# Kernel optimization log

Measured on AMD Instinct MI355X. Metric: run time of the kernel, lower is better.

Reference implementation:

```python
import jax, jax.numpy as jnp
import numpy as np

N = 4_194_304        # total nodes in the batch
NUM_GRAPHS = 32_768  # number of graphs (segments)
VOCAB = 100          # Embedding(100, 1)

# Wigner-3j contraction constants (real basis)
C01 = float(1.0 / np.sqrt(3.0))   # 0e x 1e -> 1e and 1e x 0e -> 1e
C11 = float(1.0 / np.sqrt(6.0))   # 1e x 1e -> 1e (Levi-Civita / sqrt(6))
# path weights: sqrt(ir_out.dim / fan_in_paths); 3 paths -> 1.0, 2 paths -> sqrt(3/2)
PW1 = 1.0
PW2 = float(np.sqrt(1.5))


def setup_inputs() -> dict:
    key = jax.random.key(0)
    ks = jax.random.split(key, 12)
    z = jax.random.randint(ks[0], (N,), 0, VOCAB, dtype=jnp.int32)
    pos = jax.random.normal(ks[1], (N, 3), dtype=jnp.float32)
    batch = jnp.sort(jax.random.randint(ks[2], (N,), 0, NUM_GRAPHS, dtype=jnp.int32))
    embed_table = jax.random.normal(ks[3], (VOCAB, 1), dtype=jnp.float32)
    lin_w = jax.random.normal(ks[4], (3, 3), dtype=jnp.float32) / np.sqrt(3.0)
    lin_b = jax.random.normal(ks[5], (3,), dtype=jnp.float32) * 0.1
    tp1_w = jax.random.normal(ks[6], (3,), dtype=jnp.float32)   # 3 CG paths
    tp2_w = jax.random.normal(ks[7], (2,), dtype=jnp.float32)   # 2 CG paths
    tp3_w = jax.random.normal(ks[8], (2,), dtype=jnp.float32)
    gate_w = jax.random.normal(ks[9], (2,), dtype=jnp.float32)
    fc_w = jax.random.normal(ks[10], (3, 3), dtype=jnp.float32) / np.sqrt(3.0)
    fc_b = jax.random.normal(ks[11], (3,), dtype=jnp.float32) * 0.1
    return {"z": z, "pos": pos, "batch": batch, "embed_table": embed_table,
            "lin_w": lin_w, "lin_b": lin_b, "tp1_w": tp1_w, "tp2_w": tp2_w,
            "tp3_w": tp3_w, "gate_w": gate_w, "fc_w": fc_w, "fc_b": fc_b}


def reference(z, pos, batch, embed_table, lin_w, lin_b, tp1_w, tp2_w, tp3_w, gate_w, fc_w, fc_b):
    # node features: x = [scalar embedding s (0e), transformed position v (1e)]
    s = embed_table[z][:, 0]                      # [N]
    v = pos @ lin_w.T + lin_b                     # [N, 3]
    sv = s[:, None] * v                           # [N, 3]

    # layer 1: FullyConnectedTP(x, x -> 1e); paths (0e,1e), (1e,0e), (1e,1e)
    # note: cross(v, v) == 0 structurally, kept for faithfulness to the module
    out = PW1 * (tp1_w[0] * C01 * sv
                 + tp1_w[1] * C01 * sv
                 + tp1_w[2] * C11 * jnp.cross(v, v))

    # layers 2, 3 and gate: FullyConnectedTP(out (1e), x (0e+1e) -> 1e)
    for w in (tp2_w, tp3_w, gate_w):
        out = PW2 * (w[0] * C01 * out * s[:, None]
                     + w[1] * C11 * jnp.cross(out, v))

    out = out @ fc_w.T + fc_b                     # [N, 3]
    return jax.ops.segment_sum(out, batch, num_segments=NUM_GRAPHS)  # [G, 3]
```

## Files before the change

### kernel.cpp

```cpp
#include <hip/hip_runtime.h>

#define BLOCK 256
#define NPT 8
#define CHUNK (BLOCK * NPT)

__global__ __launch_bounds__(256) void zero_out(float4* __restrict__ out, int n4) {
    int i = blockIdx.x * blockDim.x + threadIdx.x;
    if (i < n4) out[i] = make_float4(0.f, 0.f, 0.f, 0.f);
}

__global__ __launch_bounds__(BLOCK) void e3nn_fused(
    const int* __restrict__ z, const float* __restrict__ pos,
    const int* __restrict__ batch,
    const float* __restrict__ embed,
    const float* __restrict__ lin_w, const float* __restrict__ lin_b,
    const float* __restrict__ tp1_w, const float* __restrict__ tp2_w,
    const float* __restrict__ tp3_w, const float* __restrict__ gate_w,
    const float* __restrict__ fc_w, const float* __restrict__ fc_b,
    float* __restrict__ out, int n)
{
    __shared__ float t4[128];

    const int tid = threadIdx.x;
    const int lane = tid & 63;

    if (tid < 100) {
        float e = embed[tid];
        float e2 = e * e;
        t4[tid] = e2 * e2;
    }
    __syncthreads();

    const long long i0 = (long long)blockIdx.x * CHUNK + (long long)tid * NPT;

    float px[NPT], py[NPT], pz[NPT];
    int zi[NPT], bi[NPT];

    if (i0 + NPT <= (long long)n) {
        const float4* p4 = (const float4*)(pos + i0 * 3);
        float4 q0 = p4[0], q1 = p4[1], q2 = p4[2], q3 = p4[3], q4 = p4[4], q5 = p4[5];
        px[0]=q0.x; py[0]=q0.y; pz[0]=q0.z;
        px[1]=q0.w; py[1]=q1.x; pz[1]=q1.y;
        px[2]=q1.z; py[2]=q1.w; pz[2]=q2.x;
        px[3]=q2.y; py[3]=q2.z; pz[3]=q2.w;
        px[4]=q3.x; py[4]=q3.y; pz[4]=q3.z;
        px[5]=q3.w; py[5]=q4.x; pz[5]=q4.y;
        px[6]=q4.z; py[6]=q4.w; pz[6]=q5.x;
        px[7]=q5.y; py[7]=q5.z; pz[7]=q5.w;
        int4 za = *(const int4*)(z + i0), zb = *(const int4*)(z + i0 + 4);
        zi[0]=za.x; zi[1]=za.y; zi[2]=za.z; zi[3]=za.w;
        zi[4]=zb.x; zi[5]=zb.y; zi[6]=zb.z; zi[7]=zb.w;
        int4 ba = *(const int4*)(batch + i0), bb = *(const int4*)(batch + i0 + 4);
        bi[0]=ba.x; bi[1]=ba.y; bi[2]=ba.z; bi[3]=ba.w;
        bi[4]=bb.x; bi[5]=bb.y; bi[6]=bb.z; bi[7]=bb.w;
    } else {
#pragma unroll
        for (int k = 0; k < NPT; ++k) {
            long long i = i0 + k;
            if (i < (long long)n) {
                px[k]=pos[i*3]; py[k]=pos[i*3+1]; pz[k]=pos[i*3+2];
                zi[k]=z[i]; bi[k]=batch[i];
            } else { px[k]=0.f; py[k]=0.f; pz[k]=0.f; zi[k]=0; bi[k]=-1; }
        }
    }

    const float C01 = 0.57735026918962576f;
    const float PW2 = 1.2247448713915890f;
    const float k1  = (tp1_w[0] + tp1_w[1]) * C01;
    const float C   = k1 * (PW2*tp2_w[0]*C01) * (PW2*tp3_w[0]*C01) * (PW2*gate_w[0]*C01);

    float lw[9], fw[9], lbv[3], fbv[3];
#pragma unroll
    for (int i = 0; i < 9; ++i) { lw[i] = lin_w[i]; fw[i] = fc_w[i]; }
#pragma unroll
    for (int i = 0; i < 3; ++i) { lbv[i] = lin_b[i]; fbv[i] = fc_b[i]; }

    float W[9], u[3];
#pragma unroll
    for (int r = 0; r < 3; ++r) {
#pragma unroll
        for (int cc = 0; cc < 3; ++cc)
            W[r*3+cc] = fw[r*3+0]*lw[0*3+cc] + fw[r*3+1]*lw[1*3+cc] + fw[r*3+2]*lw[2*3+cc];
        u[r] = fw[r*3+0]*lbv[0] + fw[r*3+1]*lbv[1] + fw[r*3+2]*lbv[2];
    }

    auto flush = [&](int g, float ax, float ay, float az, float at, float cnt) {
        float yx = C * (W[0]*ax + W[1]*ay + W[2]*az + at*u[0]) + cnt*fbv[0];
        float yy = C * (W[3]*ax + W[4]*ay + W[5]*az + at*u[1]) + cnt*fbv[1];
        float yz = C * (W[6]*ax + W[7]*ay + W[8]*az + at*u[2]) + cnt*fbv[2];
        atomicAdd(&out[(long long)g*3+0], yx);
        atomicAdd(&out[(long long)g*3+1], yy);
        atomicAdd(&out[(long long)g*3+2], yz);
    };

    float ax=0.f, ay=0.f, az=0.f, at=0.f, ac=0.f;
    int rb = -1;

#pragma unroll
    for (int k = 0; k < NPT; ++k) {
        if (bi[k] < 0) continue;
        float t = t4[zi[k]];
        if (bi[k] == rb) {
            ax += t*px[k]; ay += t*py[k]; az += t*pz[k]; at += t; ac += 1.f;
        } else {
            if (rb >= 0) flush(rb, ax, ay, az, at, ac);
            rb = bi[k];
            ax = t*px[k]; ay = t*py[k]; az = t*pz[k]; at = t; ac = 1.f;
        }
    }

#pragma unroll
    for (int off = 1; off < 64; off <<= 1) {
        int   ob = __shfl_down(rb, off);
        float qx = __shfl_down(ax, off);
        float qy = __shfl_down(ay, off);
        float qz = __shfl_down(az, off);
        float qt = __shfl_down(at, off);
        float qc = __shfl_down(ac, off);
        if ((lane + off) < 64 && ob == rb) {
            ax += qx; ay += qy; az += qz; at += qt; ac += qc;
        }
    }
    int pb = __shfl_up(rb, 1);
    bool head = (lane == 0) || (pb != rb);
    if (rb >= 0 && head) flush(rb, ax, ay, az, at, ac);
}

extern "C" void kernel_launch(void* const* d_in, const int* in_sizes, int n_in,
                              void* d_out, int out_size, void* d_ws, size_t ws_size,
                              hipStream_t stream) {
    const int*   z     = (const int*)  d_in[0];
    const float* pos   = (const float*)d_in[1];
    const int*   batch = (const int*)  d_in[2];
    const float* embed = (const float*)d_in[3];
    const float* lin_w = (const float*)d_in[4];
    const float* lin_b = (const float*)d_in[5];
    const float* tp1_w = (const float*)d_in[6];
    const float* tp2_w = (const float*)d_in[7];
    const float* tp3_w = (const float*)d_in[8];
    const float* gate_w= (const float*)d_in[9];
    const float* fc_w  = (const float*)d_in[10];
    const float* fc_b  = (const float*)d_in[11];
    float* out = (float*)d_out;

    int n = in_sizes[0];

    int n4 = out_size / 4;
    zero_out<<<(n4 + 255) / 256, 256, 0, stream>>>((float4*)out, n4);

    int nblocks = (n + CHUNK - 1) / CHUNK;
    e3nn_fused<<<nblocks, BLOCK, 0, stream>>>(
        z, pos, batch, embed, lin_w, lin_b,
        tp1_w, tp2_w, tp3_w, gate_w, fc_w, fc_b, out, n);
}
```

Baseline: 25.67 us.

## Replace global atomics and zero kernel with block-owned segment ownership and shared accumulation

```diff
diff --git a/kernel.cpp b/kernel.cpp
--- a/kernel.cpp
+++ b/kernel.cpp
@@ -3,36 +3,34 @@
 #define BLOCK 256
 #define NPT 8
 #define CHUNK (BLOCK * NPT)
-
-__global__ __launch_bounds__(256) void zero_out(float4* __restrict__ out, int n4) {
-    int i = blockIdx.x * blockDim.x + threadIdx.x;
-    if (i < n4) out[i] = make_float4(0.f, 0.f, 0.f, 0.f);
-}
-
-__global__ __launch_bounds__(BLOCK) void e3nn_fused(
+#define TBL 64
+
+__global__ __launch_bounds__(BLOCK) void e3nn_one(
     const int* __restrict__ z, const float* __restrict__ pos,
-    const int* __restrict__ batch,
-    const float* __restrict__ embed,
+    const int* __restrict__ batch, const float* __restrict__ embed,
     const float* __restrict__ lin_w, const float* __restrict__ lin_b,
     const float* __restrict__ tp1_w, const float* __restrict__ tp2_w,
     const float* __restrict__ tp3_w, const float* __restrict__ gate_w,
     const float* __restrict__ fc_w, const float* __restrict__ fc_b,
-    float* __restrict__ out, int n)
+    float* __restrict__ out, int n, int G)
 {
-    __shared__ float t4[128];
-
-    const int tid = threadIdx.x;
+    __shared__ float t4[100];
+    __shared__ float acc[TBL * 5];
+
+    const int tid  = threadIdx.x;
     const int lane = tid & 63;
-
-    if (tid < 100) {
-        float e = embed[tid];
-        float e2 = e * e;
-        t4[tid] = e2 * e2;
-    }
+    const int b    = blockIdx.x;
+    const int s    = b * CHUNK;
+    const int e    = min(s + CHUNK, n);
+
+    if (tid < 100) { float v = embed[tid]; float v2 = v * v; t4[tid] = v2 * v2; }
+    for (int i = tid; i < TBL * 5; i += BLOCK) acc[i] = 0.f;
     __syncthreads();
 
-    const long long i0 = (long long)blockIdx.x * CHUNK + (long long)tid * NPT;
-
+    const int prev   = (s == 0) ? -1 : batch[s - 1];
+    const int mylast = batch[e - 1];
+
+    const long long i0 = (long long)s + (long long)tid * NPT;
     float px[NPT], py[NPT], pz[NPT];
     int zi[NPT], bi[NPT];
 
@@ -64,38 +62,19 @@
         }
     }
 
-    const float C01 = 0.57735026918962576f;
-    const float PW2 = 1.2247448713915890f;
-    const float k1  = (tp1_w[0] + tp1_w[1]) * C01;
-    const float C   = k1 * (PW2*tp2_w[0]*C01) * (PW2*tp3_w[0]*C01) * (PW2*gate_w[0]*C01);
-
-    float lw[9], fw[9], lbv[3], fbv[3];
-#pragma unroll
-    for (int i = 0; i < 9; ++i) { lw[i] = lin_w[i]; fw[i] = fc_w[i]; }
-#pragma unroll
-    for (int i = 0; i < 3; ++i) { lbv[i] = lin_b[i]; fbv[i] = fc_b[i]; }
-
-    float W[9], u[3];
-#pragma unroll
-    for (int r = 0; r < 3; ++r) {
-#pragma unroll
-        for (int cc = 0; cc < 3; ++cc)
-            W[r*3+cc] = fw[r*3+0]*lw[0*3+cc] + fw[r*3+1]*lw[1*3+cc] + fw[r*3+2]*lw[2*3+cc];
-        u[r] = fw[r*3+0]*lbv[0] + fw[r*3+1]*lbv[1] + fw[r*3+2]*lbv[2];
-    }
-
-    auto flush = [&](int g, float ax, float ay, float az, float at, float cnt) {
-        float yx = C * (W[0]*ax + W[1]*ay + W[2]*az + at*u[0]) + cnt*fbv[0];
-        float yy = C * (W[3]*ax + W[4]*ay + W[5]*az + at*u[1]) + cnt*fbv[1];
-        float yz = C * (W[6]*ax + W[7]*ay + W[8]*az + at*u[2]) + cnt*fbv[2];
-        atomicAdd(&out[(long long)g*3+0], yx);
-        atomicAdd(&out[(long long)g*3+1], yy);
-        atomicAdd(&out[(long long)g*3+2], yz);
+    auto lflush = [&](int g, float ax, float ay, float az, float at, float ac) {
+        int slot = g - prev - 1;
+        if (slot >= 0 && slot < TBL) {
+            atomicAdd(&acc[slot*5+0], ax);
+            atomicAdd(&acc[slot*5+1], ay);
+            atomicAdd(&acc[slot*5+2], az);
+            atomicAdd(&acc[slot*5+3], at);
+            atomicAdd(&acc[slot*5+4], ac);
+        }
     };
 
     float ax=0.f, ay=0.f, az=0.f, at=0.f, ac=0.f;
     int rb = -1;
-
 #pragma unroll
     for (int k = 0; k < NPT; ++k) {
         if (bi[k] < 0) continue;
@@ -103,7 +82,7 @@
         if (bi[k] == rb) {
             ax += t*px[k]; ay += t*py[k]; az += t*pz[k]; at += t; ac += 1.f;
         } else {
-            if (rb >= 0) flush(rb, ax, ay, az, at, ac);
+            if (rb >= 0) lflush(rb, ax, ay, az, at, ac);
             rb = bi[k];
             ax = t*px[k]; ay = t*py[k]; az = t*pz[k]; at = t; ac = 1.f;
         }
@@ -121,9 +100,87 @@
             ax += qx; ay += qy; az += qz; at += qt; ac += qc;
         }
     }
-    int pb = __shfl_up(rb, 1);
-    bool head = (lane == 0) || (pb != rb);
-    if (rb >= 0 && head) flush(rb, ax, ay, az, at, ac);
+    {
+        int pb = __shfl_up(rb, 1);
+        bool head = (lane == 0) || (pb != rb);
+        if (rb >= 0 && head) lflush(rb, ax, ay, az, at, ac);
+    }
+
+    if ((tid >> 6) == 3 && e < n && mylast > prev) {
+        float sx=0.f, sy=0.f, sz=0.f, st=0.f, sc=0.f;
+        int base = e;
+        for (;;) {
+            bool allok = true;
+#pragma unroll
+            for (int k = 0; k < 4; ++k) {
+                int idx = base + lane * 4 + k;
+                bool ok = (idx < n) && (batch[idx] == mylast);
+                if (ok) {
+                    float t = t4[z[idx]];
+                    sx += t*pos[3*idx]; sy += t*pos[3*idx+1]; sz += t*pos[3*idx+2];
+                    st += t; sc += 1.f;
+                } else allok = false;
+            }
+            unsigned long long m = __ballot(allok);
+            if (m != ~0ULL) break;
+            base += 256;
+        }
+#pragma unroll
+        for (int off = 1; off < 64; off <<= 1) {
+            sx += __shfl_xor(sx, off);
+            sy += __shfl_xor(sy, off);
+            sz += __shfl_xor(sz, off);
+            st += __shfl_xor(st, off);
+            sc += __shfl_xor(sc, off);
+        }
+        if (lane == 0) {
+            int slot = mylast - prev - 1;
+            if (slot < TBL) {
+                atomicAdd(&acc[slot*5+0], sx);
+                atomicAdd(&acc[slot*5+1], sy);
+                atomicAdd(&acc[slot*5+2], sz);
+                atomicAdd(&acc[slot*5+3], st);
+                atomicAdd(&acc[slot*5+4], sc);
+            }
+        }
+    }
+
+    __syncthreads();
+
+    const float C01 = 0.57735026918962576f;
+    const float PW2 = 1.2247448713915890f;
+    const float k1  = (tp1_w[0] + tp1_w[1]) * C01;
+    const float C   = k1 * (PW2*tp2_w[0]*C01) * (PW2*tp3_w[0]*C01) * (PW2*gate_w[0]*C01);
+
+    float lw[9], fw[9], lbv[3], fbv[3];
+#pragma unroll
+    for (int i = 0; i < 9; ++i) { lw[i] = lin_w[i]; fw[i] = fc_w[i]; }
+#pragma unroll
+    for (int i = 0; i < 3; ++i) { lbv[i] = lin_b[i]; fbv[i] = fc_b[i]; }
+
+    float W[9], u[3];
+#pragma unroll
+    for (int r = 0; r < 3; ++r) {
+#pragma unroll
+        for (int cc = 0; cc < 3; ++cc)
+            W[r*3+cc] = fw[r*3+0]*lw[0*3+cc] + fw[r*3+1]*lw[1*3+cc] + fw[r*3+2]*lw[2*3+cc];
+        u[r] = fw[r*3+0]*lbv[0] + fw[r*3+1]*lbv[1] + fw[r*3+2]*lbv[2];
+    }
+
+    const int gend  = (e == n) ? (G - 1) : mylast;
+    const int count = gend - prev;
+
+    for (int o = tid; o < count; o += BLOCK) {
+        float vx=0.f, vy=0.f, vz=0.f, vt=0.f, vc=0.f;
+        if (o < TBL) {
+            vx = acc[o*5+0]; vy = acc[o*5+1]; vz = acc[o*5+2];
+            vt = acc[o*5+3]; vc = acc[o*5+4];
+        }
+        int g = prev + 1 + o;
+        out[3*g+0] = C * (W[0]*vx + W[1]*vy + W[2]*vz + vt*u[0]) + vc*fbv[0];
+        out[3*g+1] = C * (W[3]*vx + W[4]*vy + W[5]*vz + vt*u[1]) + vc*fbv[1];
+        out[3*g+2] = C * (W[6]*vx + W[7]*vy + W[8]*vz + vt*u[2]) + vc*fbv[2];
+    }
 }
 
 extern "C" void kernel_launch(void* const* d_in, const int* in_sizes, int n_in,
@@ -144,12 +201,10 @@
     float* out = (float*)d_out;
 
     int n = in_sizes[0];
-
-    int n4 = out_size / 4;
-    zero_out<<<(n4 + 255) / 256, 256, 0, stream>>>((float4*)out, n4);
+    int G = out_size / 3;
 
     int nblocks = (n + CHUNK - 1) / CHUNK;
-    e3nn_fused<<<nblocks, BLOCK, 0, stream>>>(
+    e3nn_one<<<nblocks, BLOCK, 0, stream>>>(
         z, pos, batch, embed, lin_w, lin_b,
-        tp1_w, tp2_w, tp3_w, gate_w, fc_w, fc_b, out, n);
+        tp1_w, tp2_w, tp3_w, gate_w, fc_w, fc_b, out, n, G);
 }
```

After: 22.54 us. 1.14x faster.
